# Kernel optimization log

Measured on AMD Instinct MI355X. Metric: run time of the kernel, lower is better.

## Reference

```python
import jax, jax.numpy as jnp
import numpy as np

CH = 512
RED = CH // 8  # 64


def setup_inputs() -> dict:
    key = jax.random.key(0)
    ks = jax.random.split(key, 8)
    s = 0.05
    x = jax.random.normal(ks[0], (4, CH, 64, 64), dtype=jnp.float32)
    Wq = jax.random.normal(ks[1], (RED, CH), dtype=jnp.float32) * s
    bq = jnp.zeros((RED,), dtype=jnp.float32)
    Wk = jax.random.normal(ks[2], (RED, CH), dtype=jnp.float32) * s
    bk = jnp.zeros((RED,), dtype=jnp.float32)
    Wv = jax.random.normal(ks[3], (CH, CH), dtype=jnp.float32) * s
    bv = jnp.zeros((CH,), dtype=jnp.float32)
    gamma = jnp.zeros((1,), dtype=jnp.float32)
    return {"x": x, "Wq": Wq, "bq": bq, "Wk": Wk, "bk": bk, "Wv": Wv, "bv": bv, "gamma": gamma}


def reference(x, Wq, bq, Wk, bk, Wv, bv, gamma):
    b, c, h, w = x.shape
    n = h * w
    xf = x.reshape(b, c, n)  # [b, c, n]
    # 1x1 convs == per-pixel linear over channels
    q = jnp.einsum('rc,bcn->bnr', Wq, xf) + bq[None, None, :]   # [b, n, red]
    k = jnp.einsum('rc,bcn->brn', Wk, xf) + bk[None, :, None]   # [b, red, n]
    v = jnp.einsum('oc,bcn->bon', Wv, xf) + bv[None, :, None]   # [b, c, n]
    energy = jnp.einsum('bnr,brm->bnm', q, k)                   # [b, n, n]
    attention = jax.nn.softmax(energy, axis=-1)
    # out[b,c,i] = sum_j v[b,c,j] * attention[b,i,j]
    out = jnp.einsum('bcj,bij->bci', v, attention).reshape(b, c, h, w)
    return gamma[0] * out + x
```

## Files before the change

kernel.cpp:

```cpp
#include <hip/hip_runtime.h>
#include <math.h>

#define CH 512
#define RED 64

typedef __attribute__((ext_vector_type(4))) float f32x4;
typedef long i64;

typedef const __attribute__((address_space(1))) void* gas_t;
typedef __attribute__((address_space(3))) void* las_t;

static __device__ __forceinline__ void gl16(const void* g, void* l) {
    __builtin_amdgcn_global_load_lds((gas_t)g, (las_t)l, 16, 0, 0);
}

static __device__ __forceinline__ unsigned pk4(float a, float b, float c, float d) {
    int w = __builtin_amdgcn_cvt_pk_fp8_f32(a, b, 0, false);
    w = __builtin_amdgcn_cvt_pk_fp8_f32(c, d, w, true);
    return (unsigned)w;
}
static __device__ __forceinline__ unsigned char pk1(float a) {
    return (unsigned char)(__builtin_amdgcn_cvt_pk_fp8_f32(a, a, 0, false) & 0xFF);
}

static __device__ __forceinline__ float fexp2(float v) {
#if __has_builtin(__builtin_amdgcn_exp2f)
    return __builtin_amdgcn_exp2f(v);
#else
    float r; asm("v_exp_f32 %0, %1" : "=v"(r) : "v"(v)); return r;
#endif
}

static __device__ __forceinline__ void barrier_raw() {
    asm volatile("" ::: "memory");
    __builtin_amdgcn_s_barrier();
    asm volatile("" ::: "memory");
}

__global__ __launch_bounds__(128) void prep_w(
    const float* __restrict__ Wq, const float* __restrict__ Wk,
    const float* __restrict__ Wv, unsigned char* __restrict__ Wcat)
{
    const int r = blockIdx.x, t = threadIdx.x;
    const float* src = (r < 64) ? (Wq + (size_t)r * CH)
                     : (r < 128) ? (Wk + (size_t)(r - 64) * CH)
                                 : (Wv + (size_t)(r - 128) * CH);
    const float4 v = *(const float4*)&src[t * 4];
    *(unsigned*)&Wcat[(size_t)r * CH + t * 4] = pk4(v.x, v.y, v.z, v.w);
}

__global__ __launch_bounds__(256) void cast_xt(
    const float* __restrict__ x, unsigned char* __restrict__ xT, int n)
{
    __shared__ float sX[64][65];
    const int b = blockIdx.z, i0 = blockIdx.x * 64, c0 = blockIdx.y * 64;
    const int t = threadIdx.x;
    #pragma unroll
    for (int s = 0; s < 4; ++s) {
        const int id = s * 256 + t, c = id >> 4, seg = id & 15;
        *(float4*)&sX[c][seg * 4] = *(const float4*)&x[((size_t)b * CH + c0 + c) * n + i0 + seg * 4];
    }
    __syncthreads();
    const int i = t >> 2, cp = t & 3;
    uint4 w;
    w.x = pk4(sX[cp*16+ 0][i], sX[cp*16+ 1][i], sX[cp*16+ 2][i], sX[cp*16+ 3][i]);
    w.y = pk4(sX[cp*16+ 4][i], sX[cp*16+ 5][i], sX[cp*16+ 6][i], sX[cp*16+ 7][i]);
    w.z = pk4(sX[cp*16+ 8][i], sX[cp*16+ 9][i], sX[cp*16+10][i], sX[cp*16+11][i]);
    w.w = pk4(sX[cp*16+12][i], sX[cp*16+13][i], sX[cp*16+14][i], sX[cp*16+15][i]);
    *(uint4*)&xT[((size_t)b * n + i0 + i) * CH + c0 + cp * 16] = w;
}

__global__ __launch_bounds__(256, 4) void qkv_gemm(
    const unsigned char* __restrict__ xT, const unsigned char* __restrict__ Wcat,
    const float* __restrict__ bq, const float* __restrict__ bk,
    const float* __restrict__ bv,
    unsigned char* __restrict__ qF, unsigned char* __restrict__ kF,
    unsigned char* __restrict__ v2, int n)
{
    __shared__ char smem[20480];
    const int b = blockIdx.z, i0 = blockIdx.x * 128, o0 = blockIdx.y * 128;
    const int t = threadIdx.x, lane = t & 63;
    const int quad = lane >> 4, l16 = lane & 15;
    const int wrow = (t >> 6) & 1, wcol = t >> 7;

    f32x4 acc[4][4];
    const f32x4 zz = {0.f, 0.f, 0.f, 0.f};
    #pragma unroll
    for (int mi = 0; mi < 4; ++mi)
        #pragma unroll
        for (int ci = 0; ci < 4; ++ci) acc[mi][ci] = zz;

    const unsigned char* Ab = xT + ((size_t)b * n + i0) * CH;
    const unsigned char* Bb = Wcat + (size_t)o0 * CH;

    for (int c0 = 0; c0 < CH; c0 += 64) {
        #pragma unroll
        for (int s = 0; s < 5; ++s) {
            const int c = s * 256 + t;
            const bool isA = c < 640;
            const int tc = isA ? c : c - 640;
            const int r = tc / 5, p = (tc % 5) & 3;
            gl16((isA ? Ab : Bb) + (size_t)r * CH + c0 + p * 16,
                 smem + (isA ? 0 : 10240) + (size_t)tc * 16);
        }
        __syncthreads();
        #pragma unroll
        for (int kk = 0; kk < 64; kk += 32) {
            i64 af[4], bf[4];
            #pragma unroll
            for (int mi = 0; mi < 4; ++mi)
                af[mi] = *(const i64*)(smem + (wrow * 64 + mi * 16 + l16) * 80 + kk + quad * 8);
            #pragma unroll
            for (int ci = 0; ci < 4; ++ci)
                bf[ci] = *(const i64*)(smem + 10240 + (wcol * 64 + ci * 16 + l16) * 80 + kk + quad * 8);
            #pragma unroll
            for (int mi = 0; mi < 4; ++mi)
                #pragma unroll
                for (int ci = 0; ci < 4; ++ci)
                    acc[mi][ci] = __builtin_amdgcn_mfma_f32_16x16x32_fp8_fp8(af[mi], bf[ci], acc[mi][ci], 0, 0, 0);
        }
        __syncthreads();
    }

    float bb[4], scl[4];
    #pragma unroll
    for (int ci = 0; ci < 4; ++ci) {
        const int o = wcol * 64 + ci * 16 + l16;
        if (o0 == 0) {
            bb[ci]  = (o < 64) ? bq[o] : bk[o - 64];
            scl[ci] = (o < 64) ? 1.44269504088896f : 1.0f;
        } else {
            bb[ci]  = bv[o0 - 128 + o];
            scl[ci] = 1.0f;
        }
    }
    __syncthreads();
    unsigned char* sE = (unsigned char*)smem;
    if (o0 == 0) {
        #pragma unroll
        for (int mi = 0; mi < 4; ++mi)
            #pragma unroll
            for (int ci = 0; ci < 4; ++ci)
                #pragma unroll
                for (int r = 0; r < 4; ++r)
                    sE[(wrow*64 + mi*16 + quad*4 + r) * 144 + wcol*64 + ci*16 + l16] =
                        pk1((acc[mi][ci][r] + bb[ci]) * scl[ci]);
    } else {
        #pragma unroll
        for (int mi = 0; mi < 4; ++mi)
            #pragma unroll
            for (int ci = 0; ci < 4; ++ci)
                #pragma unroll
                for (int r = 0; r < 4; ++r)
                    sE[(wcol*64 + ci*16 + l16) * 144 + wrow*64 + mi*16 + quad*4 + r] =
                        pk1(acc[mi][ci][r] + bb[ci]);
    }
    __syncthreads();
    if (o0 == 0) {
        #pragma unroll
        for (int u = 0; u < 2; ++u) {
            const int id = u * 256 + t, i = id >> 2, p = id & 3;
            *(uint4*)&qF[((size_t)b * n + i0 + i) * RED + p * 16] = *(const uint4*)&sE[i * 144 + p * 16];
        }
        #pragma unroll
        for (int u = 0; u < 2; ++u) {
            const int id = u * 256 + t, i = id >> 2, p = id & 3;
            *(uint4*)&kF[((size_t)b * n + i0 + i) * RED + p * 16] = *(const uint4*)&sE[i * 144 + 64 + p * 16];
        }
    } else {
        #pragma unroll
        for (int u = 0; u < 4; ++u) {
            const int id = u * 256 + t, o = id >> 3, p = id & 7;
            *(uint4*)&v2[((size_t)b * CH + (o0 - 128) + o) * n + i0 + p * 16] =
                *(const uint4*)&sE[o * 144 + p * 16];
        }
    }
}

#define STGSZ 20480
#define SPOFF 40960
#define SLOFF 45056

#define CHUNK(BASE, cc) do {                                                  \
    f32x4 S0 = zz, S1 = zz;                                                   \
    __builtin_amdgcn_s_setprio(1);                                            \
    {                                                                         \
        const i64 kf0 = *(const i64*)(smem + (BASE) + fA);                    \
        const i64 kf1 = *(const i64*)(smem + (BASE) + (fA ^ 32));             \
        S0 = __builtin_amdgcn_mfma_f32_16x16x32_fp8_fp8(kf0, qreg[0][0], S0, 0, 0, 0); \
        S1 = __builtin_amdgcn_mfma_f32_16x16x32_fp8_fp8(kf0, qreg[1][0], S1, 0, 0, 0); \
        S0 = __builtin_amdgcn_mfma_f32_16x16x32_fp8_fp8(kf1, qreg[0][1], S0, 0, 0, 0); \
        S1 = __builtin_amdgcn_mfma_f32_16x16x32_fp8_fp8(kf1, qreg[1][1], S1, 0, 0, 0); \
    }                                                                         \
    __builtin_amdgcn_s_setprio(0);                                            \
      \
    float c0 = fmaxf(fmaxf(S0[0], S0[1]), fmaxf(S0[2], S0[3]));               \
    float c1 = fmaxf(fmaxf(S1[0], S1[1]), fmaxf(S1[2], S1[3]));               \
    c0 = fmaxf(c0, __shfl_xor(c0, 16)); c0 = fmaxf(c0, __shfl_xor(c0, 32));   \
    c1 = fmaxf(c1, __shfl_xor(c1, 16)); c1 = fmaxf(c1, __shfl_xor(c1, 32));   \
    if (quad == 0) {                                                          \
        *(float*)(smem + mxW) = c0;                                           \
        *(float*)(smem + mxW + 256) = c1;                                     \
    }                                                                         \
    asm volatile("s_waitcnt lgkmcnt(0)" ::: "memory");                        \
    barrier_raw();                          \
    {                                                                         \
        const f32x4 mx0 = *(const f32x4*)(smem + mxR);                        \
        const f32x4 mx1 = *(const f32x4*)(smem + mxR + 256);                  \
        const float cd0 = fmaxf(fmaxf(mx0[0], mx0[1]), fmaxf(mx0[2], mx0[3]));\
        const float cd1 = fmaxf(fmaxf(mx1[0], mx1[1]), fmaxf(mx1[2], mx1[3]));\
        const float mn0 = fmaxf(mold[0], cd0), mn1 = fmaxf(mold[1], cd1);     \
        const float rs0 = fexp2(mold[0] - mn0), rs1 = fexp2(mold[1] - mn1);   \
        mold[0] = mn0; mold[1] = mn1;                                         \
        const float e00 = fexp2(S0[0] - mn0), e01 = fexp2(S0[1] - mn0);       \
        const float e02 = fexp2(S0[2] - mn0), e03 = fexp2(S0[3] - mn0);       \
        lacc[0] = lacc[0] * rs0 + ((e00 + e01) + (e02 + e03));                \
        *(unsigned*)(smem + pwA) = pk4(e00, e01, e02, e03);                   \
        const float e10 = fexp2(S1[0] - mn1), e11 = fexp2(S1[1] - mn1);       \
        const float e12 = fexp2(S1[2] - mn1), e13 = fexp2(S1[3] - mn1);       \
        lacc[1] = lacc[1] * rs1 + ((e10 + e11) + (e12 + e13));                \
        *(unsigned*)(smem + pwA + 1024) = pk4(e10, e11, e12, e13);            \
        _Pragma("unroll")                                                     \
        for (int ct = 0; ct < 4; ++ct)                                        \
            _Pragma("unroll")                                                 \
            for (int rr = 0; rr < 4; ++rr) {                                  \
                acc[0][ct][rr] *= rs0;                                        \
                acc[1][ct][rr] *= rs1;                                        \
            }                                                                 \
    }                                                                         \
    asm volatile("s_waitcnt lgkmcnt(0)" ::: "memory");                        \
    barrier_raw();         \
    __builtin_amdgcn_s_setprio(1);                                            \
    _Pragma("unroll")                                                         \
    for (int kki = 0; kki < 2; ++kki) {                                       \
        const int kx = kki << 5;                                              \
        i64 vf_[4], pf_[2];                                                   \
        _Pragma("unroll")                                                     \
        for (int ct = 0; ct < 4; ++ct)                                        \
            vf_[ct] = *(const i64*)(smem + (BASE) + (vA ^ kx) + ct * 1024);   \
        _Pragma("unroll")                                                     \
        for (int qt = 0; qt < 2; ++qt)                                        \
            pf_[qt] = *(const i64*)(smem + (pA ^ kx) + qt * 1024);            \
        _Pragma("unroll")                                                     \
        for (int qt = 0; qt < 2; ++qt)                                        \
            _Pragma("unroll")                                                 \
            for (int ct = 0; ct < 4; ++ct)                                    \
                acc[qt][ct] = __builtin_amdgcn_mfma_f32_16x16x32_fp8_fp8(vf_[ct], pf_[qt], acc[qt][ct], 0, 0, 0); \
    }                                                                         \
    __builtin_amdgcn_s_setprio(0);                                            \
    asm volatile("s_waitcnt lgkmcnt(0)" ::: "memory");                        \
    barrier_raw();                    \
    if ((cc) + 2 < nchunks) {                                                 \
        if (t < 256) gl16(kP, smem + (BASE) + kDstOff);                       \
        gl16(vP0, smem + (BASE) + vDstOff0);                                  \
        gl16(vP1, smem + (BASE) + vDstOff1);                                  \
        kP += 4096; vP0 += 64; vP1 += 64;                                     \
        if (w < 4) asm volatile("s_waitcnt vmcnt(3)" ::: "memory");           \
        else       asm volatile("s_waitcnt vmcnt(2)" ::: "memory");           \
        __builtin_amdgcn_sched_barrier(0);                                    \
        barrier_raw();                    \
    } else if ((cc) + 1 < nchunks) {                                          \
        asm volatile("s_waitcnt vmcnt(0)" ::: "memory");                      \
        __builtin_amdgcn_sched_barrier(0);                                    \
        barrier_raw();                                                        \
    }                                                                         \
} while (0)

__global__ __launch_bounds__(512, 4) void attn(
    const unsigned char* __restrict__ qF,
    const unsigned char* __restrict__ kF,
    const unsigned char* __restrict__ v2,
    const float* __restrict__ x, const float* __restrict__ gamma,
    float* __restrict__ y, int n)
{
    __shared__ char smem[46080];
    const int b = blockIdx.x >> 1, ch0 = (blockIdx.x & 1) * 256;
    const int i0 = blockIdx.y * 64;
    const int t = threadIdx.x, lane = t & 63, w = t >> 6;
    const int quad = lane >> 4, l16 = lane & 15;
    const int qh = w & 1, g = w >> 1;
    const int sw = (l16 >> 1) & 3;
    const int boff = (quad & 1) * 8;
    const int phalf = quad >> 1;
    const int p0 = phalf ^ sw;

    const int fA  = (g * 16 + l16) * 64 + p0 * 16 + boff;
    const int vA  = 4096 + (g * 64 + l16) * 64 + p0 * 16 + boff;
    const int pA  = SPOFF + (qh * 32 + l16) * 64 + p0 * 16 + boff;
    const int pwA = SPOFF + (qh * 32 + l16) * 64 + (g ^ sw) * 16 + quad * 4;
    const int mxR = SLOFF + qh * 512 + l16 * 16;
    const int mxW = mxR + g * 4;

    const unsigned char* Qb = qF + ((size_t)b * n + i0) * RED;
    const unsigned char* Kb = kF + (size_t)b * n * RED;
    const unsigned char* Vb = v2 + ((size_t)b * CH + ch0) * n;

    const int r = t >> 2, s4 = t & 3, gs = s4 ^ ((r >> 1) & 3);
    const int kDstOff  = t * 16;
    const int vDstOff0 = 4096 + t * 16;
    const int vDstOff1 = 12288 + t * 16;
    const size_t vHalf = (size_t)128 * n;
    const unsigned char* kSrc0 = Kb + (size_t)r * RED + gs * 16;
    const unsigned char* vSrc0 = Vb + (size_t)r * n + gs * 16;

    if (t < 256) {
        gl16(Qb + (size_t)r * RED + gs * 16, smem + SPOFF + kDstOff);
        gl16(kSrc0, smem + kDstOff);
    }
    gl16(vSrc0, smem + vDstOff0);
    gl16(vSrc0 + vHalf, smem + vDstOff1);
    __syncthreads();

    i64 qreg[2][2];
    #pragma unroll
    for (int qt = 0; qt < 2; ++qt) {
        #pragma unroll
        for (int kki = 0; kki < 2; ++kki)
            qreg[qt][kki] = *(const i64*)(smem + ((pA ^ (kki << 5)) + qt * 1024));
    }
    asm volatile("s_waitcnt lgkmcnt(0)" ::: "memory");
    barrier_raw();

    const int nchunks = n >> 6;
    if (nchunks > 1) {
        if (t < 256) gl16(kSrc0 + 4096, smem + STGSZ + kDstOff);
        gl16(vSrc0 + 64, smem + STGSZ + vDstOff0);
        gl16(vSrc0 + vHalf + 64, smem + STGSZ + vDstOff1);
    }
    const unsigned char* kP  = kSrc0 + 8192;
    const unsigned char* vP0 = vSrc0 + 128;
    const unsigned char* vP1 = vSrc0 + vHalf + 128;

    f32x4 acc[2][4];
    const f32x4 zz = {0.f, 0.f, 0.f, 0.f};
    #pragma unroll
    for (int qt = 0; qt < 2; ++qt)
        #pragma unroll
        for (int ct = 0; ct < 4; ++ct) acc[qt][ct] = zz;
    float lacc[2] = {0.f, 0.f};
    float mold[2] = {-3.0e38f, -3.0e38f};

    for (int c = 0; c < nchunks; c += 2) {
        CHUNK(0, c);
        CHUNK(STGSZ, c + 1);
    }

    float* sL = (float*)(smem + SLOFF);
    #pragma unroll
    for (int qt = 0; qt < 2; ++qt) {
        float v = lacc[qt];
        v += __shfl_xor(v, 16);
        v += __shfl_xor(v, 32);
        lacc[qt] = v;
    }
    __syncthreads();
    if (quad == 0) {
        #pragma unroll
        for (int qt = 0; qt < 2; ++qt) sL[w * 32 + qt * 16 + l16] = lacc[qt];
    }
    __syncthreads();
    float il[2];
    #pragma unroll
    for (int qt = 0; qt < 2; ++qt) {
        const int idx = qt * 16 + l16;
        il[qt] = 1.0f / (sL[qh * 32 + idx] + sL[(2 + qh) * 32 + idx] +
                         sL[(4 + qh) * 32 + idx] + sL[(6 + qh) * 32 + idx]);
    }

    const float gm = gamma[0];
    float* sT = (float*)smem;
    #pragma unroll
    for (int cr = 0; cr < 4; ++cr) {
        __syncthreads();
        if (g == cr) {
            #pragma unroll
            for (int ct = 0; ct < 4; ++ct)
                #pragma unroll
                for (int qt = 0; qt < 2; ++qt)
                    #pragma unroll
                    for (int rr = 0; rr < 4; ++rr)
                        sT[(ct * 16 + quad * 4 + rr) * 68 + qh * 32 + qt * 16 + l16] =
                            acc[qt][ct][rr] * il[qt];
        }
        __syncthreads();
        const int row = t >> 3, seg = (t & 7) * 8;
        const size_t gb = ((size_t)b * CH + ch0 + cr * 64 + row) * n + i0 + seg;
        #pragma unroll
        for (int u = 0; u < 2; ++u) {
            const float4 xv = *(const float4*)&x[gb + u * 4];
            const float* op = &sT[row * 68 + seg + u * 4];
            float4 yv;
            yv.x = gm * op[0] + xv.x;
            yv.y = gm * op[1] + xv.y;
            yv.z = gm * op[2] + xv.z;
            yv.w = gm * op[3] + xv.w;
            *(float4*)&y[gb + u * 4] = yv;
        }
    }
}

extern "C" void kernel_launch(void* const* d_in, const int* in_sizes, int n_in,
                              void* d_out, int out_size, void* d_ws, size_t ws_size,
                              hipStream_t stream) {
    const float* x     = (const float*)d_in[0];
    const float* Wq    = (const float*)d_in[1];
    const float* bq    = (const float*)d_in[2];
    const float* Wk    = (const float*)d_in[3];
    const float* bk    = (const float*)d_in[4];
    const float* Wv    = (const float*)d_in[5];
    const float* bv    = (const float*)d_in[6];
    const float* gamma = (const float*)d_in[7];
    float* y = (float*)d_out;

    const int N = 64 * 64;
    const int B = in_sizes[0] / (CH * N);

    char* ws = (char*)d_ws;
    unsigned char* xT   = (unsigned char*)ws;  ws += (size_t)B * N * CH;
    unsigned char* qF   = (unsigned char*)ws;  ws += (size_t)B * N * RED;
    unsigned char* kF   = (unsigned char*)ws;  ws += (size_t)B * N * RED;
    unsigned char* v2   = (unsigned char*)ws;  ws += (size_t)B * CH * N;
    unsigned char* Wcat = (unsigned char*)ws;

    prep_w<<<dim3(640), 128, 0, stream>>>(Wq, Wk, Wv, Wcat);
    cast_xt<<<dim3(N / 64, CH / 64, B), 256, 0, stream>>>(x, xT, N);
    qkv_gemm<<<dim3(N / 128, 5, B), 256, 0, stream>>>(xT, Wcat, bq, bk, bv, qF, kF, v2, N);
    attn<<<dim3(2 * B, N / 64), 512, 0, stream>>>(qF, kF, v2, x, gamma, y, N);
}
```

Before: 227.5 us.

## Add lazy softmax rescaling with block-wide threshold vote to skip rescale

The flash-attention chunk loop now computes exponentials against the stale running max and votes, per wave and then block-wide through shared-memory flags, on whether any row's new max exceeds the old max by more than a threshold. Only when the vote fires does it update the max, recompute the exponentials, rescale the accumulators and take the second barrier. Otherwise it just adds the row sums. This removes the accumulator rescale and one barrier in most chunks. The costs are a ballot, flag stores and reads, and unscaled exponentials up to 2^4 that must still fit in fp8.

```diff
diff --git a/kernel.cpp b/kernel.cpp
--- a/kernel.cpp
+++ b/kernel.cpp
@@ -180,6 +180,8 @@
 #define STGSZ 20480
 #define SPOFF 40960
 #define SLOFF 45056
+#define FLGO  46080
+#define THRV  4.0f
 
 #define CHUNK(BASE, cc) do {                                                  \
     f32x4 S0 = zz, S1 = zz;                                                   \
@@ -193,18 +195,36 @@
         S1 = __builtin_amdgcn_mfma_f32_16x16x32_fp8_fp8(kf1, qreg[1][1], S1, 0, 0, 0); \
     }                                                                         \
     __builtin_amdgcn_s_setprio(0);                                            \
-      \
+          \
     float c0 = fmaxf(fmaxf(S0[0], S0[1]), fmaxf(S0[2], S0[3]));               \
     float c1 = fmaxf(fmaxf(S1[0], S1[1]), fmaxf(S1[2], S1[3]));               \
+    const bool predl = (c0 > mold[0] + THRV) || (c1 > mold[1] + THRV);        \
+    const unsigned long long ball = __ballot(predl);                          \
+    if (lane == 0) *(unsigned*)(smem + FLGO + w * 4) = (ball != 0ull) ? 1u : 0u; \
     c0 = fmaxf(c0, __shfl_xor(c0, 16)); c0 = fmaxf(c0, __shfl_xor(c0, 32));   \
     c1 = fmaxf(c1, __shfl_xor(c1, 16)); c1 = fmaxf(c1, __shfl_xor(c1, 32));   \
     if (quad == 0) {                                                          \
         *(float*)(smem + mxW) = c0;                                           \
         *(float*)(smem + mxW + 256) = c1;                                     \
     }                                                                         \
+         \
+    float es0, es1;                                                           \
+    {                                                                         \
+        const float e0 = fexp2(S0[0] - mold[0]), e1 = fexp2(S0[1] - mold[0]); \
+        const float e2 = fexp2(S0[2] - mold[0]), e3 = fexp2(S0[3] - mold[0]); \
+        es0 = (e0 + e1) + (e2 + e3);                                          \
+        *(unsigned*)(smem + pwA) = pk4(e0, e1, e2, e3);                       \
+        const float f0 = fexp2(S1[0] - mold[1]), f1 = fexp2(S1[1] - mold[1]); \
+        const float f2 = fexp2(S1[2] - mold[1]), f3 = fexp2(S1[3] - mold[1]); \
+        es1 = (f0 + f1) + (f2 + f3);                                          \
+        *(unsigned*)(smem + pwA + 1024) = pk4(f0, f1, f2, f3);                \
+    }                                                                         \
     asm volatile("s_waitcnt lgkmcnt(0)" ::: "memory");                        \
-    barrier_raw();                          \
-    {                                                                         \
+    barrier_raw();        \
+    const uint4 fw0 = *(const uint4*)(smem + FLGO);                           \
+    const uint4 fw1 = *(const uint4*)(smem + FLGO + 16);                      \
+    if (fw0.x | fw0.y | fw0.z | fw0.w | fw1.x | fw1.y | fw1.z | fw1.w) {      \
+             \
         const f32x4 mx0 = *(const f32x4*)(smem + mxR);                        \
         const f32x4 mx1 = *(const f32x4*)(smem + mxR + 256);                  \
         const float cd0 = fmaxf(fmaxf(mx0[0], mx0[1]), fmaxf(mx0[2], mx0[3]));\
@@ -212,14 +232,14 @@
         const float mn0 = fmaxf(mold[0], cd0), mn1 = fmaxf(mold[1], cd1);     \
         const float rs0 = fexp2(mold[0] - mn0), rs1 = fexp2(mold[1] - mn1);   \
         mold[0] = mn0; mold[1] = mn1;                                         \
-        const float e00 = fexp2(S0[0] - mn0), e01 = fexp2(S0[1] - mn0);       \
-        const float e02 = fexp2(S0[2] - mn0), e03 = fexp2(S0[3] - mn0);       \
-        lacc[0] = lacc[0] * rs0 + ((e00 + e01) + (e02 + e03));                \
-        *(unsigned*)(smem + pwA) = pk4(e00, e01, e02, e03);                   \
-        const float e10 = fexp2(S1[0] - mn1), e11 = fexp2(S1[1] - mn1);       \
-        const float e12 = fexp2(S1[2] - mn1), e13 = fexp2(S1[3] - mn1);       \
-        lacc[1] = lacc[1] * rs1 + ((e10 + e11) + (e12 + e13));                \
-        *(unsigned*)(smem + pwA + 1024) = pk4(e10, e11, e12, e13);            \
+        const float e0 = fexp2(S0[0] - mn0), e1 = fexp2(S0[1] - mn0);         \
+        const float e2 = fexp2(S0[2] - mn0), e3 = fexp2(S0[3] - mn0);         \
+        lacc[0] = lacc[0] * rs0 + ((e0 + e1) + (e2 + e3));                    \
+        *(unsigned*)(smem + pwA) = pk4(e0, e1, e2, e3);                       \
+        const float f0 = fexp2(S1[0] - mn1), f1 = fexp2(S1[1] - mn1);         \
+        const float f2 = fexp2(S1[2] - mn1), f3 = fexp2(S1[3] - mn1);         \
+        lacc[1] = lacc[1] * rs1 + ((f0 + f1) + (f2 + f3));                    \
+        *(unsigned*)(smem + pwA + 1024) = pk4(f0, f1, f2, f3);                \
         _Pragma("unroll")                                                     \
         for (int ct = 0; ct < 4; ++ct)                                        \
             _Pragma("unroll")                                                 \
@@ -227,9 +247,11 @@
                 acc[0][ct][rr] *= rs0;                                        \
                 acc[1][ct][rr] *= rs1;                                        \
             }                                                                 \
-    }                                                                         \
-    asm volatile("s_waitcnt lgkmcnt(0)" ::: "memory");                        \
-    barrier_raw();         \
+        asm volatile("s_waitcnt lgkmcnt(0)" ::: "memory");                    \
+        barrier_raw();         \
+    } else {                                                                  \
+        lacc[0] += es0; lacc[1] += es1;                                       \
+    }                                                                         \
     __builtin_amdgcn_s_setprio(1);                                            \
     _Pragma("unroll")                                                         \
     for (int kki = 0; kki < 2; ++kki) {                                       \
@@ -273,7 +295,7 @@
     const float* __restrict__ x, const float* __restrict__ gamma,
     float* __restrict__ y, int n)
 {
-    __shared__ char smem[46080];
+    __shared__ char smem[46336];
     const int b = blockIdx.x >> 1, ch0 = (blockIdx.x & 1) * 256;
     const int i0 = blockIdx.y * 64;
     const int t = threadIdx.x, lane = t & 63, w = t >> 6;
```

Result: slower. 241.9 us (+6.3%).
